# Kernel tuning notes

Measured on AMD Instinct MI355X. Metric: run time of the kernel, lower is better.

## Reference

```python
import jax, jax.numpy as jnp
import numpy as np
import math

# (mul, l, parity) triples for irreps_in1 == irreps_in2 == '32x0e+16x1o+8x2e'
IRREPS = [(32, 0, 1), (16, 1, -1), (8, 2, 1)]
BATCH = 2048


def _fact(n):
    return math.factorial(n)


def _w3j_entry(j1, j2, j3, m1, m2, m3):
    # Racah formula for the (complex-basis) Wigner 3j symbol, integer l's.
    if m1 + m2 + m3 != 0:
        return 0.0
    t_min = max(0, j2 - j3 - m1, j1 - j3 + m2)
    t_max = min(j1 + j2 - j3, j1 - m1, j2 + m2)
    if t_max < t_min:
        return 0.0
    s = 0.0
    for t in range(t_min, t_max + 1):
        s += (-1) ** t / (
            _fact(t) * _fact(j3 - j2 + t + m1) * _fact(j3 - j1 + t - m2)
            * _fact(j1 + j2 - j3 - t) * _fact(j1 - t - m1) * _fact(j2 - t + m2))
    delta = math.sqrt(_fact(j1 + j2 - j3) * _fact(j1 - j2 + j3)
                      * _fact(-j1 + j2 + j3) / _fact(j1 + j2 + j3 + 1))
    pref = math.sqrt(_fact(j1 + m1) * _fact(j1 - m1) * _fact(j2 + m2)
                     * _fact(j2 - m2) * _fact(j3 + m3) * _fact(j3 - m3))
    return (-1) ** (j1 - j2 - m3) * delta * pref * s


def _w3j_complex(j1, j2, j3):
    W = np.zeros((2 * j1 + 1, 2 * j2 + 1, 2 * j3 + 1))
    for m1 in range(-j1, j1 + 1):
        for m2 in range(-j2, j2 + 1):
            m3 = -(m1 + m2)
            if abs(m3) <= j3:
                W[m1 + j1, m2 + j2, m3 + j3] = _w3j_entry(j1, j2, j3, m1, m2, m3)
    return W


def _c2r(l):
    # complex -> real spherical harmonic change-of-basis (rows: real m, cols: complex mu)
    U = np.zeros((2 * l + 1, 2 * l + 1), dtype=np.complex128)
    U[l, l] = 1.0
    rs2 = 1.0 / math.sqrt(2.0)
    for m in range(1, l + 1):
        U[l + m, l + m] = (-1) ** m * rs2
        U[l + m, l - m] = rs2
        U[l - m, l - m] = 1j * rs2
        U[l - m, l + m] = -1j * (-1) ** m * rs2
    return U


def _w3j_real(l1, l2, l3):
    # Wigner 3j in the real spherical-harmonic basis (same sparsity/math as e3nn o3.wigner_3j)
    W = _w3j_complex(l1, l2, l3).astype(np.complex128)
    C = np.einsum('abc,ia,jb,kc->ijk', W, _c2r(l1), _c2r(l2), _c2r(l3))
    if np.linalg.norm(C.imag) > np.linalg.norm(C.real):
        C = np.ascontiguousarray(C.imag)
    else:
        C = np.ascontiguousarray(C.real)
    C[np.abs(C) < 1e-12] = 0.0
    return C


def _build_structure():
    # Mirrors CudaTensorProduct.__init__ with irreps_out=None: enumerate every
    # then emit sparse COO entries (in1_idx, in2_idx, out_idx, cb_val).
    entries_by_l3 = {}
    off1 = 0
    for mul1, l1, p1 in IRREPS:
        off2_base = 0
        for mul2, l2, p2 in IRREPS:
            for l3 in range(abs(l1 - l2), l1 + l2 + 1):
                p3 = (p1 * p2 + 1) // 2
                o1 = off1
                for _i in range(mul1):
                    o2 = off2_base
                    for _j in range(mul2):
                        entries_by_l3.setdefault((l3, p3), []).append((l1, l2, o1, o2))
                        o2 += 2 * l2 + 1
                    o1 += 2 * l1 + 1
            off2_base += (2 * l2 + 1) * mul2
        off1 += (2 * l1 + 1) * mul1

    l3s = sorted(entries_by_l3.keys(), key=lambda x: 2 * (x[0] + 1) + x[1])
    in1_idx, in2_idx, out_idx, cb_vals = [], [], [], []
    row = 0
    w3j_cache = {}
    for l3, p3 in l3s:
        for l1, l2, o1, o2 in entries_by_l3[(l3, p3)]:
            key = (l1, l2, l3)
            if key not in w3j_cache:
                w3j_cache[key] = _w3j_real(l1, l2, l3)
            C = w3j_cache[key]
            scale = math.sqrt(2 * l3 + 1)
            for m3 in range(2 * l3 + 1):
                for m2 in range(2 * l2 + 1):
                    for m1 in range(2 * l1 + 1):
                        v = C[m1, m2, m3]
                        if v == 0.0:
                            continue
                        in1_idx.append(m1 + o1)
                        in2_idx.append(m2 + o2)
                        out_idx.append(m3 + row)
                        cb_vals.append(float(v * scale))
            row += 2 * l3 + 1

    # palette/index encoding, as in the module (palette[0] == 0 is the filler slot)
    palette = sorted(set(cb_vals))
    palette.insert(0, 0.0)
    lut = {v: i for i, v in enumerate(palette)}
    cb_idx = [lut[v] for v in cb_vals]
    return (np.asarray(in1_idx, np.int32), np.asarray(in2_idx, np.int32),
            np.asarray(out_idx, np.int32), np.asarray(cb_idx, np.int32),
            np.asarray(palette, np.float32), row)


def setup_inputs() -> dict:
    key = jax.random.key(0)
    k1, k2 = jax.random.split(key)
    i1, i2, io, ic, pal, cb_height = _build_structure()
    dim = sum(m * (2 * l + 1) for m, l, _ in IRREPS)  # 120
    return {
        'in1': jax.random.normal(k1, (BATCH, dim), jnp.float32),
        'in2': jax.random.normal(k2, (BATCH, dim), jnp.float32),
        'cb_palette': jnp.asarray(pal),
        'in1_indices': jnp.asarray(i1),
        'in2_indices': jnp.asarray(i2),
        'out_indices': jnp.asarray(io),
        'cb_indices': jnp.asarray(ic),
        'cb_height': int(cb_height),
    }


def reference(in1, in2, cb_palette, in1_indices, in2_indices, out_indices, cb_indices, cb_height):
    # intermediate[b, o] = sum_k palette[cb_idx[k]] * in1[b, i1[k]] * in2[b, i2[k]]
    vals = cb_palette[cb_indices]                                   # [K]
    contrib = in1[:, in1_indices] * in2[:, in2_indices] * vals[None, :]  # [B, K]
    # scatter-accumulate along the sparse output rows
    out = jax.ops.segment_sum(contrib.T, out_indices, num_segments=cb_height).T  # [B, cb_height]
    return out
```

## Files before the change

kernel.cpp:

```cpp
#include <hip/hip_runtime.h>

#define DIM 120
#define NB 16
#define NBP 20
#define BLOCK 256
#define NG (NB / 4)
#define NXCD 8
#define SMEM_FLOATS (2 * DIM * NBP)

typedef float f32x4 __attribute__((ext_vector_type(4)));

__global__ void pre_kernel(const int* __restrict__ oi, int K, int H,
                           int* __restrict__ row_start,
                           const int* __restrict__ i1, const int* __restrict__ i2,
                           const int* __restrict__ cb, const float* __restrict__ pal,
                           uint2* __restrict__ ent) {
    int k = blockIdx.x * blockDim.x + threadIdx.x;
    if (k < K) {
        uint2 e;
        e.x = (unsigned)i1[k] | ((unsigned)i2[k] << 16);
        e.y = __float_as_uint(pal[cb[k]]);
        ent[k] = e;
        const int cur = oi[k];
        const int prev = (k == 0) ? -1 : oi[k - 1];
        for (int o = prev + 1; o <= cur; ++o) row_start[o] = k;
    } else if (k == K) {
        const int prev = oi[K - 1];
        for (int o = prev + 1; o <= H; ++o) row_start[o] = K;
    }
}

__global__ __launch_bounds__(BLOCK, 8) void tp_kernel(
    const float* __restrict__ in1, const float* __restrict__ in2,
    const uint2* __restrict__ ent, const int* __restrict__ row_start,
    float* __restrict__ out, int H, int nbx) {
    int x = blockIdx.x;
    {
        const int q = nbx / NXCD, r = nbx % NXCD;
        const int xcd = x % NXCD, pos = x / NXCD;
        x = (xcd < r) ? (xcd * (q + 1) + pos) : (r * (q + 1) + (xcd - r) * q + pos);
    }

    __shared__ __align__(16) float smem[SMEM_FLOATS];
    float* __restrict__ s1t = smem;
    float* __restrict__ s2t = smem + DIM * NBP;

    const int b0 = blockIdx.y * NB;
    for (int t = threadIdx.x; t < 2 * DIM * NG; t += BLOCK) {
        const int arr = (t >= DIM * NG);
        const int c = arr ? t - DIM * NG : t;
        const int d = c % DIM;
        const int g = c / DIM;
        const float* __restrict__ src = arr ? in2 : in1;
        const size_t base = (size_t)(b0 + 4 * g) * DIM + d;
        float4 v;
        v.x = src[base + 0 * DIM];
        v.y = src[base + 1 * DIM];
        v.z = src[base + 2 * DIM];
        v.w = src[base + 3 * DIM];
        float* dst = arr ? s2t : s1t;
        *(float4*)(dst + d * NBP + 4 * g) = v;
    }
    __syncthreads();

    const int o0 = x * BLOCK;
    const int o = o0 + (int)threadIdx.x;
    const bool act = (o < H);

    float acc[NB];
#pragma unroll
    for (int b = 0; b < NB; ++b) acc[b] = 0.0f;

    if (act) {
        const int k0 = row_start[o];
        const int k1 = row_start[o + 1];
        for (int k = k0; k < k1; ++k) {
            const uint2 e = ent[k];
            const float4* __restrict__ pa = (const float4*)(s1t + (e.x & 0xffffu) * NBP);
            const float4* __restrict__ pc = (const float4*)(s2t + (e.x >> 16) * NBP);
            const float v = __uint_as_float(e.y);
#pragma unroll
            for (int j = 0; j < NG; ++j) {
                const float4 x4 = pa[j];
                const float4 y4 = pc[j];
                acc[4 * j + 0] = fmaf(v * x4.x, y4.x, acc[4 * j + 0]);
                acc[4 * j + 1] = fmaf(v * x4.y, y4.y, acc[4 * j + 1]);
                acc[4 * j + 2] = fmaf(v * x4.z, y4.z, acc[4 * j + 2]);
                acc[4 * j + 3] = fmaf(v * x4.w, y4.w, acc[4 * j + 3]);
            }
        }
    }
    __syncthreads();

    if (o0 + BLOCK <= H) {
#pragma unroll
        for (int b = 0; b < NB; ++b)
            smem[b * BLOCK + threadIdx.x] = acc[b];
        __syncthreads();
        const int wave = threadIdx.x >> 6;
        const int lane = threadIdx.x & 63;
        f32x4 vv[NB / 4];
#pragma unroll
        for (int it = 0; it < NB / 4; ++it)
            vv[it] = *(const f32x4*)(smem + (it * 4 + wave) * BLOCK + 4 * lane);
#pragma unroll
        for (int it = 0; it < NB / 4; ++it)
            __builtin_nontemporal_store(
                vv[it],
                (f32x4*)(out + (size_t)(b0 + it * 4 + wave) * H + o0 + 4 * lane));
    } else if (act) {
#pragma unroll
        for (int b = 0; b < NB; ++b)
            __builtin_nontemporal_store(acc[b], &out[(size_t)(b0 + b) * H + o]);
    }
}

extern "C" void kernel_launch(void* const* d_in, const int* in_sizes, int n_in,
                              void* d_out, int out_size, void* d_ws, size_t ws_size,
                              hipStream_t stream) {
    const float* in1 = (const float*)d_in[0];
    const float* in2 = (const float*)d_in[1];
    const float* pal = (const float*)d_in[2];
    const int*   i1  = (const int*)d_in[3];
    const int*   i2  = (const int*)d_in[4];
    const int*   oi  = (const int*)d_in[5];
    const int*   cb  = (const int*)d_in[6];

    const int K = in_sizes[3];
    const int B = in_sizes[0] / DIM;
    const int H = out_size / B;

    uint2* ent = (uint2*)d_ws;
    int* row_start = (int*)((char*)d_ws + (size_t)K * sizeof(uint2));

    pre_kernel<<<(K + 1 + 255) / 256, 256, 0, stream>>>(oi, K, H, row_start,
                                                        i1, i2, cb, pal, ent);

    const int nbx = (H + BLOCK - 1) / BLOCK;
    dim3 grid(nbx, B / NB);
    tp_kernel<<<grid, BLOCK, 0, stream>>>(in1, in2, ent, row_start,
                                          (float*)d_out, H, nbx);
}
```

Baseline: 30.71 us.

## Fuse preprocessing into main kernel with per-block row-start search in LDS

Removes the separate pre_kernel launch and computes row start offsets inside each block. It does this with a two-level ballot-based search over out_indices and fills a shared-memory row_start table. The palette is staged into LDS, and i1/i2/cb are read directly instead of from a packed entry array. This trades one kernel launch and a global round trip for redundant per-block search work, extra syncs, and three separate index loads per nonzero. It also fails if the palette has more than 256 entries.

```diff
diff --git a/kernel.cpp b/kernel.cpp
--- a/kernel.cpp
+++ b/kernel.cpp
@@ -7,46 +7,38 @@
 #define NG (NB / 4)
 #define NXCD 8
 #define SMEM_FLOATS (2 * DIM * NBP)
+#define PAL_MAX 256
 
 typedef float f32x4 __attribute__((ext_vector_type(4)));
 
-__global__ void pre_kernel(const int* __restrict__ oi, int K, int H,
-                           int* __restrict__ row_start,
-                           const int* __restrict__ i1, const int* __restrict__ i2,
-                           const int* __restrict__ cb, const float* __restrict__ pal,
-                           uint2* __restrict__ ent) {
-    int k = blockIdx.x * blockDim.x + threadIdx.x;
-    if (k < K) {
-        uint2 e;
-        e.x = (unsigned)i1[k] | ((unsigned)i2[k] << 16);
-        e.y = __float_as_uint(pal[cb[k]]);
-        ent[k] = e;
-        const int cur = oi[k];
-        const int prev = (k == 0) ? -1 : oi[k - 1];
-        for (int o = prev + 1; o <= cur; ++o) row_start[o] = k;
-    } else if (k == K) {
-        const int prev = oi[K - 1];
-        for (int o = prev + 1; o <= H; ++o) row_start[o] = K;
-    }
-}
-
 __global__ __launch_bounds__(BLOCK, 8) void tp_kernel(
     const float* __restrict__ in1, const float* __restrict__ in2,
-    const uint2* __restrict__ ent, const int* __restrict__ row_start,
-    float* __restrict__ out, int H, int nbx) {
+    const float* __restrict__ pal, int paln,
+    const int* __restrict__ i1, const int* __restrict__ i2,
+    const int* __restrict__ oi, const int* __restrict__ cb,
+    float* __restrict__ out, int H, int K, int nbx) {
+    __shared__ __align__(16) float smem[SMEM_FLOATS];
+    __shared__ int rs[BLOCK + 1];
+    __shared__ float pal_lds[PAL_MAX];
+    __shared__ int cnt[4];
+
+    float* __restrict__ s1t = smem;
+    float* __restrict__ s2t = smem + DIM * NBP;
+    const int tid = threadIdx.x;
+
     int x = blockIdx.x;
     {
         const int q = nbx / NXCD, r = nbx % NXCD;
         const int xcd = x % NXCD, pos = x / NXCD;
         x = (xcd < r) ? (xcd * (q + 1) + pos) : (r * (q + 1) + (xcd - r) * q + pos);
     }
+    const int o0 = x * BLOCK;
 
-    __shared__ __align__(16) float smem[SMEM_FLOATS];
-    float* __restrict__ s1t = smem;
-    float* __restrict__ s2t = smem + DIM * NBP;
+    if (tid < 4) cnt[tid] = 0;
+    for (int t = tid; t < paln && t < PAL_MAX; t += BLOCK) pal_lds[t] = pal[t];
 
     const int b0 = blockIdx.y * NB;
-    for (int t = threadIdx.x; t < 2 * DIM * NG; t += BLOCK) {
+    for (int t = tid; t < 2 * DIM * NG; t += BLOCK) {
         const int arr = (t >= DIM * NG);
         const int c = arr ? t - DIM * NG : t;
         const int d = c % DIM;
@@ -63,8 +55,54 @@
     }
     __syncthreads();
 
-    const int o0 = x * BLOCK;
-    const int o = o0 + (int)threadIdx.x;
+    const int v1 = (o0 + BLOCK < H) ? (o0 + BLOCK) : H;
+    const int stride = (K + BLOCK - 1) / BLOCK;
+    {
+        const size_t p = (size_t)tid * stride;
+        const bool valid = p < (size_t)K;
+        const int vi = oi[valid ? p : (size_t)(K - 1)];
+        const unsigned long long m0 = __ballot(valid && (vi < o0));
+        const unsigned long long m1 = __ballot(valid && (vi < v1));
+        if ((tid & 63) == 0) {
+            atomicAdd(&cnt[0], (int)__popcll(m0));
+            atomicAdd(&cnt[1], (int)__popcll(m1));
+        }
+    }
+    __syncthreads();
+    const int c0 = cnt[0], c1 = cnt[1];
+    const int lo0 = (c0 == 0) ? 0 : (c0 - 1) * stride + 1;
+    const int lo1 = (c1 == 0) ? 0 : (c1 - 1) * stride + 1;
+    {
+        const int kk0 = lo0 + tid;
+        const int kk1 = lo1 + tid;
+        const bool p0 = (tid < stride) && (kk0 < K) && (oi[kk0] < o0);
+        const bool p1 = (tid < stride) && (kk1 < K) && (oi[kk1] < v1);
+        const unsigned long long m0 = __ballot(p0);
+        const unsigned long long m1 = __ballot(p1);
+        if ((tid & 63) == 0) {
+            atomicAdd(&cnt[2], (int)__popcll(m0));
+            atomicAdd(&cnt[3], (int)__popcll(m1));
+        }
+    }
+    __syncthreads();
+    const int k0b = lo0 + cnt[2];
+    const int k1b = lo1 + cnt[3];
+
+    for (int kk = k0b + tid; kk < k1b; kk += BLOCK) {
+        const int cur = oi[kk];
+        const int prevv = (kk == 0) ? -1 : oi[kk - 1];
+        for (int o = (prevv + 1 > o0 ? prevv + 1 : o0); o <= cur; ++o)
+            rs[o - o0] = kk;
+    }
+    if (tid == 0) {
+        const int prevv = (k1b == 0) ? -1 : oi[k1b - 1];
+        const int lo = (prevv + 1 > o0) ? prevv + 1 : o0;
+        for (int o = lo; o <= o0 + BLOCK; ++o)
+            rs[o - o0] = k1b;
+    }
+    __syncthreads();
+
+    const int o = o0 + tid;
     const bool act = (o < H);
 
     float acc[NB];
@@ -72,13 +110,14 @@
     for (int b = 0; b < NB; ++b) acc[b] = 0.0f;
 
     if (act) {
-        const int k0 = row_start[o];
-        const int k1 = row_start[o + 1];
+        const int k0 = rs[tid];
+        const int k1 = rs[tid + 1];
         for (int k = k0; k < k1; ++k) {
-            const uint2 e = ent[k];
-            const float4* __restrict__ pa = (const float4*)(s1t + (e.x & 0xffffu) * NBP);
-            const float4* __restrict__ pc = (const float4*)(s2t + (e.x >> 16) * NBP);
-            const float v = __uint_as_float(e.y);
+            const int a = i1[k];
+            const int c = i2[k];
+            const float v = pal_lds[cb[k]];
+            const float4* __restrict__ pa = (const float4*)(s1t + a * NBP);
+            const float4* __restrict__ pc = (const float4*)(s2t + c * NBP);
 #pragma unroll
             for (int j = 0; j < NG; ++j) {
                 const float4 x4 = pa[j];
@@ -95,10 +134,10 @@
     if (o0 + BLOCK <= H) {
 #pragma unroll
         for (int b = 0; b < NB; ++b)
-            smem[b * BLOCK + threadIdx.x] = acc[b];
+            smem[b * BLOCK + tid] = acc[b];
         __syncthreads();
-        const int wave = threadIdx.x >> 6;
-        const int lane = threadIdx.x & 63;
+        const int wave = tid >> 6;
+        const int lane = tid & 63;
         f32x4 vv[NB / 4];
 #pragma unroll
         for (int it = 0; it < NB / 4; ++it)
@@ -126,18 +165,13 @@
     const int*   oi  = (const int*)d_in[5];
     const int*   cb  = (const int*)d_in[6];
 
+    const int paln = in_sizes[2];
     const int K = in_sizes[3];
     const int B = in_sizes[0] / DIM;
     const int H = out_size / B;
 
-    uint2* ent = (uint2*)d_ws;
-    int* row_start = (int*)((char*)d_ws + (size_t)K * sizeof(uint2));
-
-    pre_kernel<<<(K + 1 + 255) / 256, 256, 0, stream>>>(oi, K, H, row_start,
-                                                        i1, i2, cb, pal, ent);
-
     const int nbx = (H + BLOCK - 1) / BLOCK;
     dim3 grid(nbx, B / NB);
-    tp_kernel<<<grid, BLOCK, 0, stream>>>(in1, in2, ent, row_start,
-                                          (float*)d_out, H, nbx);
+    tp_kernel<<<grid, BLOCK, 0, stream>>>(in1, in2, pal, paln, i1, i2, oi, cb,
+                                          (float*)d_out, H, K, nbx);
 }
```

New measurement: 34.72 us. 13.1% more time.

## Process multiple output tiles per block to amortize shared-memory input staging

Applied to the files above, without the earlier changes.

Each block now loops over three consecutive 256-row output tiles, reusing the staged in1/in2 shared-memory tile across them. This cuts the number of blocks and the repeated global loads of the same batch inputs. It also drops the LDS-transposed vectorized output store path in favor of direct per-element nontemporal stores, which removes barriers but gives less coalesced writes. Fewer blocks means less parallelism.

```diff
diff --git a/kernel.cpp b/kernel.cpp
--- a/kernel.cpp
+++ b/kernel.cpp
@@ -6,9 +6,7 @@
 #define BLOCK 256
 #define NG (NB / 4)
 #define NXCD 8
-#define SMEM_FLOATS (2 * DIM * NBP)
-
-typedef float f32x4 __attribute__((ext_vector_type(4)));
+#define TILES 3
 
 __global__ void pre_kernel(const int* __restrict__ oi, int K, int H,
                            int* __restrict__ row_start,
@@ -33,47 +31,45 @@
 __global__ __launch_bounds__(BLOCK, 8) void tp_kernel(
     const float* __restrict__ in1, const float* __restrict__ in2,
     const uint2* __restrict__ ent, const int* __restrict__ row_start,
-    float* __restrict__ out, int H, int nbx) {
-    int x = blockIdx.x;
+    float* __restrict__ out, int H, int ngrp) {
+    int g = blockIdx.x;
     {
-        const int q = nbx / NXCD, r = nbx % NXCD;
-        const int xcd = x % NXCD, pos = x / NXCD;
-        x = (xcd < r) ? (xcd * (q + 1) + pos) : (r * (q + 1) + (xcd - r) * q + pos);
+        const int q = ngrp / NXCD, r = ngrp % NXCD;
+        const int xcd = g % NXCD, pos = g / NXCD;
+        g = (xcd < r) ? (xcd * (q + 1) + pos) : (r * (q + 1) + (xcd - r) * q + pos);
     }
 
-    __shared__ __align__(16) float smem[SMEM_FLOATS];
-    float* __restrict__ s1t = smem;
-    float* __restrict__ s2t = smem + DIM * NBP;
+    __shared__ __align__(16) float s1t[DIM * NBP];
+    __shared__ __align__(16) float s2t[DIM * NBP];
 
     const int b0 = blockIdx.y * NB;
     for (int t = threadIdx.x; t < 2 * DIM * NG; t += BLOCK) {
         const int arr = (t >= DIM * NG);
         const int c = arr ? t - DIM * NG : t;
         const int d = c % DIM;
-        const int g = c / DIM;
+        const int gg = c / DIM;
         const float* __restrict__ src = arr ? in2 : in1;
-        const size_t base = (size_t)(b0 + 4 * g) * DIM + d;
+        const size_t base = (size_t)(b0 + 4 * gg) * DIM + d;
         float4 v;
         v.x = src[base + 0 * DIM];
         v.y = src[base + 1 * DIM];
         v.z = src[base + 2 * DIM];
         v.w = src[base + 3 * DIM];
         float* dst = arr ? s2t : s1t;
-        *(float4*)(dst + d * NBP + 4 * g) = v;
+        *(float4*)(dst + d * NBP + 4 * gg) = v;
     }
     __syncthreads();
 
-    const int o0 = x * BLOCK;
-    const int o = o0 + (int)threadIdx.x;
-    const bool act = (o < H);
-
-    float acc[NB];
-#pragma unroll
-    for (int b = 0; b < NB; ++b) acc[b] = 0.0f;
-
-    if (act) {
+    for (int t = 0; t < TILES; ++t) {
+        const int o = (g * TILES + t) * BLOCK + (int)threadIdx.x;
+        if (o >= H) continue;
         const int k0 = row_start[o];
         const int k1 = row_start[o + 1];
+
+        float acc[NB];
+#pragma unroll
+        for (int b = 0; b < NB; ++b) acc[b] = 0.0f;
+
         for (int k = k0; k < k1; ++k) {
             const uint2 e = ent[k];
             const float4* __restrict__ pa = (const float4*)(s1t + (e.x & 0xffffu) * NBP);
@@ -89,26 +85,7 @@
                 acc[4 * j + 3] = fmaf(v * x4.w, y4.w, acc[4 * j + 3]);
             }
         }
-    }
-    __syncthreads();
 
-    if (o0 + BLOCK <= H) {
-#pragma unroll
-        for (int b = 0; b < NB; ++b)
-            smem[b * BLOCK + threadIdx.x] = acc[b];
-        __syncthreads();
-        const int wave = threadIdx.x >> 6;
-        const int lane = threadIdx.x & 63;
-        f32x4 vv[NB / 4];
-#pragma unroll
-        for (int it = 0; it < NB / 4; ++it)
-            vv[it] = *(const f32x4*)(smem + (it * 4 + wave) * BLOCK + 4 * lane);
-#pragma unroll
-        for (int it = 0; it < NB / 4; ++it)
-            __builtin_nontemporal_store(
-                vv[it],
-                (f32x4*)(out + (size_t)(b0 + it * 4 + wave) * H + o0 + 4 * lane));
-    } else if (act) {
 #pragma unroll
         for (int b = 0; b < NB; ++b)
             __builtin_nontemporal_store(acc[b], &out[(size_t)(b0 + b) * H + o]);
@@ -137,7 +114,8 @@
                                                         i1, i2, cb, pal, ent);
 
     const int nbx = (H + BLOCK - 1) / BLOCK;
-    dim3 grid(nbx, B / NB);
+    const int ngrp = (nbx + TILES - 1) / TILES;
+    dim3 grid(ngrp, B / NB);
     tp_kernel<<<grid, BLOCK, 0, stream>>>(in1, in2, ent, row_start,
-                                          (float*)d_out, H, nbx);
+                                          (float*)d_out, H, ngrp);
 }
```

Measured after the change: 35.02 us. 1.14x slower.
